# Optimization experiments

Measured on AMD Instinct MI355X. Metric: run time of the kernel, lower is better.

Reference implementation:

```python
import jax, jax.numpy as jnp
import numpy as np

B, N, K = 4, 512, 10
PI_SCALE = 0.05  # keeps sum_k pi in (0, 0.5) so the [1e-8, 1] clamp does not saturate at 1
MCMC_KEY = jax.random.key(42)


def setup_inputs() -> dict:
    key = jax.random.key(0)
    k1, k2, k3, k4 = jax.random.split(key, 4)
    mu = jax.random.normal(k1, (B, N, K), dtype=jnp.float32)
    sig = jax.random.uniform(k2, (B, N, K), dtype=jnp.float32)
    pi = jax.random.uniform(k3, (B, N, K), dtype=jnp.float32) * PI_SCALE
    A_0 = jax.random.uniform(k4, (N, N), dtype=jnp.float32)
    return {"mu": mu, "sig": sig, "pi": pi, "A_0": A_0, "num_samples": 100}


def reference(mu, sig, pi, A_0, num_samples):
    b, n, k = mu.shape

    # Mixture-weighted proposal mean/std:  sum_k softmax(pi)_k * {mu,sig}_k
    component_probs = jax.nn.softmax(pi, axis=-1)          # [B,N,K]
    selected_mu = jnp.sum(component_probs * mu, axis=-1)    # [B,N]
    selected_sig = jnp.sum(component_probs * sig, axis=-1)  # [B,N]

    # edge_probs[b,i,j] = clamp(sum_k pi[b,i,k]) -- constant in j; hoisted out of the loop
    # since it depends only on pi (the torch code recomputes it every step).
    edge_probs = jnp.clip(jnp.sum(pi, axis=2), 1e-8, 1.0)[:, :, None]  # [B,N,1]
    log_ep = jnp.log(edge_probs)                                        # [B,N,1]
    log_1mep = jnp.log(1.0 - edge_probs)                                # [B,N,1]

    def log_likelihood(A):  # A: [B,N,N] -> [N]  (sum over dims 0,1 as in torch)
        return jnp.sum(A * log_ep + (1.0 - A) * log_1mep, axis=(0, 1))

    def step(carry, t):
        current_A, acc = carry
        kk = jax.random.fold_in(MCMC_KEY, t)
        k_noise, k_unif = jax.random.split(kk)
        noise = jax.random.normal(k_noise, (b, n), dtype=selected_mu.dtype)
        proposed_mu = selected_mu + noise * selected_sig              # [B,N]
        # sigmoid of rank-1 outer product: einsum('bnc,bmc->bnm') with c==1
        proposed_A = jax.nn.sigmoid(proposed_mu[:, :, None] * proposed_mu[:, None, :])
        ratio = jnp.mean(jnp.clip(jnp.exp(log_likelihood(proposed_A) - log_likelihood(current_A)), 0.0, 1.0))
        accept = jax.random.uniform(k_unif, (b,)) < ratio             # [B] bool
        current_A = jnp.where(accept[:, None, None], proposed_A, current_A)
        return (current_A, acc + current_A), None

    cur0 = jnp.broadcast_to(A_0, (b, n, n)).astype(mu.dtype)
    acc0 = jnp.zeros((b, n, n), dtype=mu.dtype)
    (_, acc), _ = jax.lax.scan(step, (cur0, acc0), jnp.arange(num_samples))
    return acc / num_samples
```

## Files before the change

### kernel.cpp

```cpp
#include <hip/hip_runtime.h>
#include <stdint.h>

#define T_STEPS 100
#define BB 4
#define NN 512
#define KK 10
#define TBTOT (T_STEPS * BB)
#define LLT_ELT ((size_t)TBTOT * NN)

__device__ __forceinline__ uint32_t rotl32(uint32_t v, int d) {
  return (v << d) | (v >> (32 - d));
}

__device__ __forceinline__ void tf2x32(uint32_t k0, uint32_t k1,
                                       uint32_t& x0, uint32_t& x1) {
  uint32_t k2 = k0 ^ k1 ^ 0x1BD11BDAu;
  x0 += k0; x1 += k1;
#define TFR(r) { x0 += x1; x1 = rotl32(x1, r); x1 ^= x0; }
  TFR(13) TFR(15) TFR(26) TFR(6)   x0 += k1; x1 += k2 + 1u;
  TFR(17) TFR(29) TFR(16) TFR(24)  x0 += k2; x1 += k0 + 2u;
  TFR(13) TFR(15) TFR(26) TFR(6)   x0 += k0; x1 += k1 + 3u;
  TFR(17) TFR(29) TFR(16) TFR(24)  x0 += k1; x1 += k2 + 4u;
  TFR(13) TFR(15) TFR(26) TFR(6)   x0 += k2; x1 += k0 + 5u;
#undef TFR
}

__device__ __forceinline__ float bits_to_u01(uint32_t bits) {
  return __fsub_rn(__uint_as_float((bits >> 9) | 0x3f800000u), 1.0f);
}

__device__ __forceinline__ float erfinv_f32(float x) {
  float w = -logf(__fmul_rn(__fsub_rn(1.0f, x), __fadd_rn(1.0f, x)));
  float p;
  if (w < 5.0f) {
    w = __fsub_rn(w, 2.5f);
    p = 2.81022636e-08f;
    p = __fadd_rn(__fmul_rn(p, w), 3.43273939e-07f);
    p = __fadd_rn(__fmul_rn(p, w), -3.5233877e-06f);
    p = __fadd_rn(__fmul_rn(p, w), -4.39150654e-06f);
    p = __fadd_rn(__fmul_rn(p, w), 0.00021858087f);
    p = __fadd_rn(__fmul_rn(p, w), -0.00125372503f);
    p = __fadd_rn(__fmul_rn(p, w), -0.00417768164f);
    p = __fadd_rn(__fmul_rn(p, w), 0.246640727f);
    p = __fadd_rn(__fmul_rn(p, w), 1.50140941f);
  } else {
    w = __fsub_rn(sqrtf(w), 3.0f);
    p = -0.000200214257f;
    p = __fadd_rn(__fmul_rn(p, w), 0.000100950558f);
    p = __fadd_rn(__fmul_rn(p, w), 0.00134934322f);
    p = __fadd_rn(__fmul_rn(p, w), -0.00367342844f);
    p = __fadd_rn(__fmul_rn(p, w), 0.00573950773f);
    p = __fadd_rn(__fmul_rn(p, w), -0.0076224613f);
    p = __fadd_rn(__fmul_rn(p, w), 0.00943887047f);
    p = __fadd_rn(__fmul_rn(p, w), 1.00167406f);
    p = __fadd_rn(__fmul_rn(p, w), 2.83297682f);
  }
  return __fmul_rn(p, x);
}

__device__ __forceinline__ float fast_sigmoid(float x) {
  float e = __expf(-x);
  return __builtin_amdgcn_rcpf(__fadd_rn(1.0f, e));
}

template <int CTRL>
__device__ __forceinline__ float dpp_add(float x) {
  int v = __builtin_amdgcn_update_dpp(0, __float_as_int(x), CTRL, 0xF, 0xF, true);
  return __fadd_rn(x, __int_as_float(v));
}
__device__ __forceinline__ float readlane_f(float x, int lane) {
  return __int_as_float(__builtin_amdgcn_readlane(__float_as_int(x), lane));
}

__global__ void prep_kernel(const float* __restrict__ mu,
                            const float* __restrict__ sig,
                            const float* __restrict__ pi,
                            float* __restrict__ sm, float* __restrict__ ss,
                            float* __restrict__ Lf) {
  int m = blockIdx.x * blockDim.x + threadIdx.x;
  if (m >= BB * NN) return;
  const float* pp = pi + m * KK;
  float mx = pp[0];
  for (int k = 1; k < KK; k++) mx = fmaxf(mx, pp[k]);
  float e[KK]; float s = 0.0f;
  for (int k = 0; k < KK; k++) { e[k] = expf(__fsub_rn(pp[k], mx)); s = __fadd_rn(s, e[k]); }
  float smv = 0.0f, ssv = 0.0f, eps = 0.0f;
  for (int k = 0; k < KK; k++) {
    float p = e[k] / s;
    smv = __fadd_rn(smv, __fmul_rn(p, mu[m * KK + k]));
    ssv = __fadd_rn(ssv, __fmul_rn(p, sig[m * KK + k]));
    eps = __fadd_rn(eps, pp[k]);
  }
  sm[m] = smv; ss[m] = ssv;
  float ep = fminf(fmaxf(eps, 1e-8f), 1.0f);
  float lep = logf(ep);
  float l1 = logf(__fsub_rn(1.0f, ep));
  Lf[m] = (float)((double)lep - (double)l1);
}

__global__ void rng_kernel(const float* __restrict__ sm,
                           const float* __restrict__ ss,
                           float* __restrict__ pm, float* __restrict__ uacc) {
  int id = blockIdx.x * blockDim.x + threadIdx.x;
  if (id >= T_STEPS * BB * NN) return;
  int t = id >> 11;
  int m = id & 2047;

  uint32_t kk0 = 0u, kk1 = (uint32_t)t;
  tf2x32(0u, 42u, kk0, kk1);
  uint32_t n0 = 0u, n1 = 0u; tf2x32(kk0, kk1, n0, n1);
  uint32_t y0 = 0u, y1 = (uint32_t)m;
  tf2x32(n0, n1, y0, y1);
  uint32_t bits = y0 ^ y1;

  float u01 = bits_to_u01(bits);
  const float lo = -0.99999994f;
  float u = fmaxf(lo, __fadd_rn(__fmul_rn(u01, 2.0f), lo));
  float z = __fmul_rn(1.41421356237309515f, erfinv_f32(u));
  pm[id] = __fadd_rn(sm[m], __fmul_rn(z, ss[m]));

  if (m < 4) {
    uint32_t u0 = 0u, u1 = 1u; tf2x32(kk0, kk1, u0, u1);
    uint32_t c0 = 0u, c1 = (uint32_t)m;
    tf2x32(u0, u1, c0, c1);
    uacc[t * 4 + m] = bits_to_u01(c0 ^ c1);
  }
}

template <int SPLIT>
__global__ __launch_bounds__(512) void ll_kernel(const float* __restrict__ pm,
                                                 const float* __restrict__ Lf,
                                                 const float* __restrict__ A0,
                                                 double* __restrict__ llt_p,
                                                 double* __restrict__ ll0_p) {
  constexpr int CH = NN / SPLIT;
  __shared__ float spm[CH];
  __shared__ float sLc[CH];
  int j = threadIdx.x;
  int bi = blockIdx.x;
  if (bi < TBTOT * SPLIT) {
    int tb = bi / SPLIT;
    int s = bi - tb * SPLIT;
    int b = tb & 3;
    int i0 = s * CH;
    if (j < CH) {
      spm[j] = pm[tb * NN + i0 + j];
      sLc[j] = Lf[b * NN + i0 + j];
    }
    float pmj = pm[tb * NN + j];
    __syncthreads();
    double acc = 0.0;
    #pragma unroll 8
    for (int i = 0; i < CH; i += 2) {
      float x0 = __fmul_rn(spm[i], pmj);
      float x1 = __fmul_rn(spm[i + 1], pmj);
      float t0 = __fmul_rn(fast_sigmoid(x0), sLc[i]);
      float t1 = __fmul_rn(fast_sigmoid(x1), sLc[i + 1]);
      acc += (double)__fadd_rn(t0, t1);
    }
    llt_p[(size_t)s * LLT_ELT + (size_t)tb * NN + j] = acc;
  } else {
    int bi2 = bi - TBTOT * SPLIT;
    int b = bi2 / SPLIT;
    int s = bi2 - b * SPLIT;
    int i0 = s * CH;
    if (j < CH) sLc[j] = Lf[b * NN + i0 + j];
    __syncthreads();
    double acc = 0.0;
    #pragma unroll 4
    for (int i = 0; i < CH; i++) {
      acc += (double)A0[(size_t)(i0 + i) * NN + j] * (double)sLc[i];
    }
    ll0_p[s * (BB * NN) + b * NN + j] = acc;
  }
}

template <int SPLIT>
__global__ __launch_bounds__(512) void combine_kernel(const double* __restrict__ llt_p,
                                                      const double* __restrict__ ll0_p,
                                                      double* __restrict__ llt,
                                                      double* __restrict__ ll0,
                                                      double* __restrict__ tsum) {
  int bi = blockIdx.x;
  int j = threadIdx.x;
  if (bi < T_STEPS) {
    double tj = 0.0;
    #pragma unroll
    for (int b = 0; b < BB; b++) {
      size_t idx = ((size_t)bi * BB + b) * NN + j;
      double a = llt_p[idx];
      #pragma unroll
      for (int s = 1; s < SPLIT; s++) a += llt_p[(size_t)s * LLT_ELT + idx];
      llt[idx] = a;
      tj += a;
    }
    tsum[(size_t)bi * NN + j] = tj;
  } else {
    #pragma unroll
    for (int b = 0; b < BB; b++) {
      int idx = b * NN + j;
      double a = ll0_p[idx];
      #pragma unroll
      for (int s = 1; s < SPLIT; s++) a += ll0_p[s * (BB * NN) + idx];
      ll0[idx] = a;
    }
  }
}

struct ChainBuf {
  double2 ll[4][4];
  double2 ts[4];
};

#define CH_LOAD(BUF, T)                                                      \
  {                                                                          \
    _Pragma("unroll")                                                        \
    for (int b = 0; b < 4; b++) {                                            \
      _Pragma("unroll")                                                      \
      for (int k = 0; k < 4; k++)                                            \
        BUF.ll[b][k] = llt2[((size_t)(T) * 4 + b) * 256 + k * 64 + g];       \
    }                                                                        \
    _Pragma("unroll")                                                        \
    for (int k = 0; k < 4; k++)                                              \
      BUF.ts[k] = tsum2[(size_t)(T) * 256 + k * 64 + g];                     \
  }

#define CH_ACC(BUF, B)                                                       \
  {                                                                          \
    _Pragma("unroll")                                                        \
    for (int k = 0; k < 4; k++) {                                            \
      C[k].x += BUF.ll[B][k].x - cur[B][k].x;                                \
      C[k].y += BUF.ll[B][k].y - cur[B][k].y;                                \
      cur[B][k] = BUF.ll[B][k];                                              \
    }                                                                        \
  }

#define CH_STEP(BUF, T)                                                      \
  {                                                                          \
    float4 ua = sua[T];                                                      \
    float e0x = fminf(__expf((float)(BUF.ts[0].x - C[0].x)), 1.0f);          \
    float e0y = fminf(__expf((float)(BUF.ts[0].y - C[0].y)), 1.0f);          \
    float e1x = fminf(__expf((float)(BUF.ts[1].x - C[1].x)), 1.0f);          \
    float e1y = fminf(__expf((float)(BUF.ts[1].y - C[1].y)), 1.0f);          \
    float e2x = fminf(__expf((float)(BUF.ts[2].x - C[2].x)), 1.0f);          \
    float e2y = fminf(__expf((float)(BUF.ts[2].y - C[2].y)), 1.0f);          \
    float e3x = fminf(__expf((float)(BUF.ts[3].x - C[3].x)), 1.0f);          \
    float e3y = fminf(__expf((float)(BUF.ts[3].y - C[3].y)), 1.0f);          \
    float ps = __fadd_rn(__fadd_rn(__fadd_rn(e0x, e0y), __fadd_rn(e1x, e1y)),\
                         __fadd_rn(__fadd_rn(e2x, e2y), __fadd_rn(e3x, e3y)));\
    ps = dpp_add<0xB1>(ps);                 \
    ps = dpp_add<0x4E>(ps);                 \
    ps = dpp_add<0x141>(ps);     \
    ps = dpp_add<0x140>(ps);     \
    float s0 = readlane_f(ps, 0), s1 = readlane_f(ps, 16);                   \
    float s2 = readlane_f(ps, 32), s3 = readlane_f(ps, 48);                  \
    float tot = __fadd_rn(__fadd_rn(s0, s1), __fadd_rn(s2, s3));             \
    float ratio = __fmul_rn(tot, 1.0f / 512.0f);                             \
    if (ua.x < ratio) { st.x = (T); CH_ACC(BUF, 0) }                         \
    if (ua.y < ratio) { st.y = (T); CH_ACC(BUF, 1) }                         \
    if (ua.z < ratio) { st.z = (T); CH_ACC(BUF, 2) }                         \
    if (ua.w < ratio) { st.w = (T); CH_ACC(BUF, 3) }                         \
    if (g == 0) sst[T] = st;                                                 \
  }

__global__ __launch_bounds__(64) void chain_kernel(const double* __restrict__ llt,
                                                   const double* __restrict__ tsum,
                                                   const double* __restrict__ ll0,
                                                   const float* __restrict__ uacc,
                                                   int* __restrict__ counts) {
  __shared__ float4 sua[T_STEPS];
  __shared__ int4 sst[T_STEPS];
  __shared__ int scnt[BB * (T_STEPS + 1)];
  int g = threadIdx.x;

  const float4* uacc4 = (const float4*)uacc;
  for (int t = g; t < T_STEPS; t += 64) sua[t] = uacc4[t];

  const double2* llt2  = (const double2*)llt;
  const double2* tsum2 = (const double2*)tsum;
  const double2* ll02  = (const double2*)ll0;

  double2 cur[4][4];
  #pragma unroll
  for (int b = 0; b < 4; b++)
    #pragma unroll
    for (int k = 0; k < 4; k++) cur[b][k] = ll02[b * 256 + k * 64 + g];
  double2 C[4];
  #pragma unroll
  for (int k = 0; k < 4; k++) {
    C[k].x = (cur[0][k].x + cur[1][k].x) + (cur[2][k].x + cur[3][k].x);
    C[k].y = (cur[0][k].y + cur[1][k].y) + (cur[2][k].y + cur[3][k].y);
  }
  int4 st = make_int4(-1, -1, -1, -1);

  ChainBuf R0, R1, R2;
  CH_LOAD(R0, 0)
  CH_LOAD(R1, 1)
  CH_LOAD(R2, 2)
  __syncthreads();

  for (int t = 0; t < 99; t += 3) {
    CH_STEP(R0, t)
    CH_LOAD(R0, t + 3)
    CH_STEP(R1, t + 1)
    if (t + 4 < T_STEPS) CH_LOAD(R1, t + 4)
    CH_STEP(R2, t + 2)
    if (t + 5 < T_STEPS) CH_LOAD(R2, t + 5)
  }
  CH_STEP(R0, 99)

  __syncthreads();
  for (int s = g; s < BB * (T_STEPS + 1); s += 64) scnt[s] = 0;
  __syncthreads();
  for (int t = g; t < T_STEPS; t += 64) {
    int4 s4 = sst[t];
    atomicAdd(&scnt[0 * (T_STEPS + 1) + s4.x + 1], 1);
    atomicAdd(&scnt[1 * (T_STEPS + 1) + s4.y + 1], 1);
    atomicAdd(&scnt[2 * (T_STEPS + 1) + s4.z + 1], 1);
    atomicAdd(&scnt[3 * (T_STEPS + 1) + s4.w + 1], 1);
  }
  __syncthreads();
  for (int s = g; s < BB * (T_STEPS + 1); s += 64) counts[s] = scnt[s];
}

__global__ __launch_bounds__(512) void out_kernel(const float* __restrict__ pm,
                                                  const float* __restrict__ A0,
                                                  const int* __restrict__ counts,
                                                  float* __restrict__ out) {
  __shared__ int scnt[T_STEPS + 1];
  int b = blockIdx.x >> 9;
  int i = blockIdx.x & 511;
  int j = threadIdx.x;
  if (j < T_STEPS + 1) scnt[j] = counts[b * (T_STEPS + 1) + j];
  __syncthreads();
  float r = (float)scnt[0] * A0[(size_t)i * NN + j];
  #pragma unroll 4
  for (int t = 0; t < T_STEPS; t++) {
    int c = scnt[t + 1];
    if (c) {
      float x = __fmul_rn(pm[(size_t)(t * BB + b) * NN + i],
                          pm[(size_t)(t * BB + b) * NN + j]);
      r += (float)c * fast_sigmoid(x);
    }
  }
  out[((size_t)b * NN + i) * NN + j] = r * 0.01f;
}

extern "C" void kernel_launch(void* const* d_in, const int* in_sizes, int n_in,
                              void* d_out, int out_size, void* d_ws, size_t ws_size,
                              hipStream_t stream) {
  const float* mu  = (const float*)d_in[0];
  const float* sig = (const float*)d_in[1];
  const float* pi  = (const float*)d_in[2];
  const float* A0  = (const float*)d_in[3];

  char* ws = (char*)d_ws;
  size_t off = 0;
  auto alloc = [&](size_t bytes) -> char* {
    char* p = ws + off;
    off += (bytes + 255) & ~(size_t)255;
    return p;
  };
  double* llt  = (double*)alloc(LLT_ELT * 8);
  double* ll0  = (double*)alloc(BB * NN * 8);
  double* tsum = (double*)alloc((size_t)T_STEPS * NN * 8);
  float*  pm   = (float*)alloc(LLT_ELT * 4);
  float*  Lf   = (float*)alloc(BB * NN * 4);
  float*  sm   = (float*)alloc(BB * NN * 4);
  float*  ssv  = (float*)alloc(BB * NN * 4);
  float*  uacc = (float*)alloc(T_STEPS * 4 * 4);
  int*    cnts = (int*)alloc(BB * (T_STEPS + 1) * 4);
  size_t fixed_end = off;
  float*  outp = (float*)d_out;

  size_t part4 = 4 * LLT_ELT * 8 + 4 * BB * NN * 8 + 1024;
  size_t part2 = 2 * LLT_ELT * 8 + 2 * BB * NN * 8 + 1024;
  int split = (ws_size >= fixed_end + part4) ? 4
            : (ws_size >= fixed_end + part2) ? 2 : 1;

  double* llt_p;
  double* ll0_p;
  if (split > 1) {
    llt_p = (double*)alloc((size_t)split * LLT_ELT * 8);
    ll0_p = (double*)alloc((size_t)split * BB * NN * 8);
  } else {
    llt_p = llt;
    ll0_p = ll0;
  }

  prep_kernel<<<8, 256, 0, stream>>>(mu, sig, pi, sm, ssv, Lf);
  rng_kernel<<<(T_STEPS * BB * NN + 255) / 256, 256, 0, stream>>>(sm, ssv, pm, uacc);
  if (split == 4) {
    ll_kernel<4><<<(TBTOT + BB) * 4, 512, 0, stream>>>(pm, Lf, A0, llt_p, ll0_p);
    combine_kernel<4><<<T_STEPS + 1, 512, 0, stream>>>(llt_p, ll0_p, llt, ll0, tsum);
  } else if (split == 2) {
    ll_kernel<2><<<(TBTOT + BB) * 2, 512, 0, stream>>>(pm, Lf, A0, llt_p, ll0_p);
    combine_kernel<2><<<T_STEPS + 1, 512, 0, stream>>>(llt_p, ll0_p, llt, ll0, tsum);
  } else {
    ll_kernel<1><<<TBTOT + BB, 512, 0, stream>>>(pm, Lf, A0, llt_p, ll0_p);
    combine_kernel<1><<<T_STEPS + 1, 512, 0, stream>>>(llt_p, ll0_p, llt, ll0, tsum);
  }
  chain_kernel<<<1, 64, 0, stream>>>(llt, tsum, ll0, uacc, cnts);
  out_kernel<<<BB * NN, 512, 0, stream>>>(pm, A0, cnts, outp);
}
```

Baseline: 154.1 us.

## Store per-step log-likelihoods as float and derive totals inside chain kernel

Log-likelihood partials and combined values are now stored as float instead of double. The separate tsum array is removed; the chain kernel instead computes per-column totals on the fly from the four batch values. The split==1 path also skips the combine kernel, since ll_kernel already writes straight into llt/ll0. This halves the memory traffic of the serial single-wavefront chain kernel and of combine, at the cost of float rounding in the stored likelihoods, which could flip accept decisions near the threshold.

```diff
diff --git a/kernel.cpp b/kernel.cpp
--- a/kernel.cpp
+++ b/kernel.cpp
@@ -7,6 +7,8 @@
 #define KK 10
 #define TBTOT (T_STEPS * BB)
 #define LLT_ELT ((size_t)TBTOT * NN)
+
+typedef float f4 __attribute__((ext_vector_type(4)));
 
 __device__ __forceinline__ uint32_t rotl32(uint32_t v, int d) {
   return (v << d) | (v >> (32 - d));
@@ -131,8 +133,8 @@
 __global__ __launch_bounds__(512) void ll_kernel(const float* __restrict__ pm,
                                                  const float* __restrict__ Lf,
                                                  const float* __restrict__ A0,
-                                                 double* __restrict__ llt_p,
-                                                 double* __restrict__ ll0_p) {
+                                                 float* __restrict__ llt_p,
+                                                 float* __restrict__ ll0_p) {
   constexpr int CH = NN / SPLIT;
   __shared__ float spm[CH];
   __shared__ float sLc[CH];
@@ -158,7 +160,7 @@
       float t1 = __fmul_rn(fast_sigmoid(x1), sLc[i + 1]);
       acc += (double)__fadd_rn(t0, t1);
     }
-    llt_p[(size_t)s * LLT_ELT + (size_t)tb * NN + j] = acc;
+    llt_p[(size_t)s * LLT_ELT + (size_t)tb * NN + j] = (float)acc;
   } else {
     int bi2 = bi - TBTOT * SPLIT;
     int b = bi2 / SPLIT;
@@ -171,101 +173,90 @@
     for (int i = 0; i < CH; i++) {
       acc += (double)A0[(size_t)(i0 + i) * NN + j] * (double)sLc[i];
     }
-    ll0_p[s * (BB * NN) + b * NN + j] = acc;
+    ll0_p[s * (BB * NN) + b * NN + j] = (float)acc;
   }
 }
 
 template <int SPLIT>
-__global__ __launch_bounds__(512) void combine_kernel(const double* __restrict__ llt_p,
-                                                      const double* __restrict__ ll0_p,
-                                                      double* __restrict__ llt,
-                                                      double* __restrict__ ll0,
-                                                      double* __restrict__ tsum) {
+__global__ __launch_bounds__(512) void combine_kernel(const float* __restrict__ llt_p,
+                                                      const float* __restrict__ ll0_p,
+                                                      float* __restrict__ llt,
+                                                      float* __restrict__ ll0) {
   int bi = blockIdx.x;
   int j = threadIdx.x;
   if (bi < T_STEPS) {
-    double tj = 0.0;
     #pragma unroll
     for (int b = 0; b < BB; b++) {
       size_t idx = ((size_t)bi * BB + b) * NN + j;
-      double a = llt_p[idx];
+      double a = (double)llt_p[idx];
       #pragma unroll
-      for (int s = 1; s < SPLIT; s++) a += llt_p[(size_t)s * LLT_ELT + idx];
-      llt[idx] = a;
-      tj += a;
-    }
-    tsum[(size_t)bi * NN + j] = tj;
+      for (int s = 1; s < SPLIT; s++) a += (double)llt_p[(size_t)s * LLT_ELT + idx];
+      llt[idx] = (float)a;
+    }
   } else {
     #pragma unroll
     for (int b = 0; b < BB; b++) {
       int idx = b * NN + j;
-      double a = ll0_p[idx];
+      double a = (double)ll0_p[idx];
       #pragma unroll
-      for (int s = 1; s < SPLIT; s++) a += ll0_p[s * (BB * NN) + idx];
-      ll0[idx] = a;
-    }
-  }
-}
-
-struct ChainBuf {
-  double2 ll[4][4];
-  double2 ts[4];
-};
-
-#define CH_LOAD(BUF, T)                                                      \
+      for (int s = 1; s < SPLIT; s++) a += (double)ll0_p[s * (BB * NN) + idx];
+      ll0[idx] = (float)a;
+    }
+  }
+}
+
+#define CH_LOADF(BUF, T)                                                     \
   {                                                                          \
     _Pragma("unroll")                                                        \
     for (int b = 0; b < 4; b++) {                                            \
       _Pragma("unroll")                                                      \
-      for (int k = 0; k < 4; k++)                                            \
-        BUF.ll[b][k] = llt2[((size_t)(T) * 4 + b) * 256 + k * 64 + g];       \
+      for (int k = 0; k < 2; k++)                                            \
+        BUF[b][k] = llt4[(((size_t)(T) * 4 + b) * 2 + k) * 64 + g];          \
     }                                                                        \
-    _Pragma("unroll")                                                        \
-    for (int k = 0; k < 4; k++)                                              \
-      BUF.ts[k] = tsum2[(size_t)(T) * 256 + k * 64 + g];                     \
-  }
-
-#define CH_ACC(BUF, B)                                                       \
+  }
+
+#define CH_ACCF(BUF, B)                                                      \
   {                                                                          \
     _Pragma("unroll")                                                        \
-    for (int k = 0; k < 4; k++) {                                            \
-      C[k].x += BUF.ll[B][k].x - cur[B][k].x;                                \
-      C[k].y += BUF.ll[B][k].y - cur[B][k].y;                                \
-      cur[B][k] = BUF.ll[B][k];                                              \
+    for (int k = 0; k < 2; k++) {                                            \
+      _Pragma("unroll")                                                      \
+      for (int c = 0; c < 4; c++)                                            \
+        C[k][c] += (double)BUF[B][k][c] - (double)cur[B][k][c];              \
+      cur[B][k] = BUF[B][k];                                                 \
     }                                                                        \
   }
 
-#define CH_STEP(BUF, T)                                                      \
+#define CH_STEPF(BUF, T)                                                     \
   {                                                                          \
     float4 ua = sua[T];                                                      \
-    float e0x = fminf(__expf((float)(BUF.ts[0].x - C[0].x)), 1.0f);          \
-    float e0y = fminf(__expf((float)(BUF.ts[0].y - C[0].y)), 1.0f);          \
-    float e1x = fminf(__expf((float)(BUF.ts[1].x - C[1].x)), 1.0f);          \
-    float e1y = fminf(__expf((float)(BUF.ts[1].y - C[1].y)), 1.0f);          \
-    float e2x = fminf(__expf((float)(BUF.ts[2].x - C[2].x)), 1.0f);          \
-    float e2y = fminf(__expf((float)(BUF.ts[2].y - C[2].y)), 1.0f);          \
-    float e3x = fminf(__expf((float)(BUF.ts[3].x - C[3].x)), 1.0f);          \
-    float e3y = fminf(__expf((float)(BUF.ts[3].y - C[3].y)), 1.0f);          \
-    float ps = __fadd_rn(__fadd_rn(__fadd_rn(e0x, e0y), __fadd_rn(e1x, e1y)),\
-                         __fadd_rn(__fadd_rn(e2x, e2y), __fadd_rn(e3x, e3y)));\
+    float ps = 0.0f;                                                         \
+    _Pragma("unroll")                                                        \
+    for (int k = 0; k < 2; k++) {                                            \
+      _Pragma("unroll")                                                      \
+      for (int c = 0; c < 4; c++) {                                          \
+        double ts = ((double)BUF[0][k][c] + (double)BUF[1][k][c]) +          \
+                    ((double)BUF[2][k][c] + (double)BUF[3][k][c]);           \
+        float e = fminf(__expf((float)(ts - C[k][c])), 1.0f);                \
+        ps = __fadd_rn(ps, e);                                               \
+      }                                                                      \
+    }                                                                        \
     ps = dpp_add<0xB1>(ps);                 \
     ps = dpp_add<0x4E>(ps);                 \
-    ps = dpp_add<0x141>(ps);     \
-    ps = dpp_add<0x140>(ps);     \
+    ps = dpp_add<0x141>(ps);        \
+    ps = dpp_add<0x140>(ps);        \
     float s0 = readlane_f(ps, 0), s1 = readlane_f(ps, 16);                   \
     float s2 = readlane_f(ps, 32), s3 = readlane_f(ps, 48);                  \
     float tot = __fadd_rn(__fadd_rn(s0, s1), __fadd_rn(s2, s3));             \
     float ratio = __fmul_rn(tot, 1.0f / 512.0f);                             \
-    if (ua.x < ratio) { st.x = (T); CH_ACC(BUF, 0) }                         \
-    if (ua.y < ratio) { st.y = (T); CH_ACC(BUF, 1) }                         \
-    if (ua.z < ratio) { st.z = (T); CH_ACC(BUF, 2) }                         \
-    if (ua.w < ratio) { st.w = (T); CH_ACC(BUF, 3) }                         \
+    if (ua.x < ratio) { st.x = (T); CH_ACCF(BUF, 0) }                        \
+    if (ua.y < ratio) { st.y = (T); CH_ACCF(BUF, 1) }                        \
+    if (ua.z < ratio) { st.z = (T); CH_ACCF(BUF, 2) }                        \
+    if (ua.w < ratio) { st.w = (T); CH_ACCF(BUF, 3) }                        \
     if (g == 0) sst[T] = st;                                                 \
   }
 
-__global__ __launch_bounds__(64) void chain_kernel(const double* __restrict__ llt,
-                                                   const double* __restrict__ tsum,
-                                                   const double* __restrict__ ll0,
+__global__ __launch_bounds__(64) void chain_kernel(const float* __restrict__ llt,
+                                                   const float* __restrict__ ll0,
                                                    const float* __restrict__ uacc,
                                                    int* __restrict__ counts) {
   __shared__ float4 sua[T_STEPS];
@@ -276,38 +267,38 @@
   const float4* uacc4 = (const float4*)uacc;
   for (int t = g; t < T_STEPS; t += 64) sua[t] = uacc4[t];
 
-  const double2* llt2  = (const double2*)llt;
-  const double2* tsum2 = (const double2*)tsum;
-  const double2* ll02  = (const double2*)ll0;
-
-  double2 cur[4][4];
+  const f4* llt4 = (const f4*)llt;
+  const f4* ll04 = (const f4*)ll0;
+
+  f4 cur[4][2];
   #pragma unroll
   for (int b = 0; b < 4; b++)
     #pragma unroll
-    for (int k = 0; k < 4; k++) cur[b][k] = ll02[b * 256 + k * 64 + g];
-  double2 C[4];
+    for (int k = 0; k < 2; k++) cur[b][k] = ll04[(b * 2 + k) * 64 + g];
+  double C[2][4];
   #pragma unroll
-  for (int k = 0; k < 4; k++) {
-    C[k].x = (cur[0][k].x + cur[1][k].x) + (cur[2][k].x + cur[3][k].x);
-    C[k].y = (cur[0][k].y + cur[1][k].y) + (cur[2][k].y + cur[3][k].y);
-  }
+  for (int k = 0; k < 2; k++)
+    #pragma unroll
+    for (int c = 0; c < 4; c++)
+      C[k][c] = ((double)cur[0][k][c] + (double)cur[1][k][c]) +
+                ((double)cur[2][k][c] + (double)cur[3][k][c]);
   int4 st = make_int4(-1, -1, -1, -1);
 
-  ChainBuf R0, R1, R2;
-  CH_LOAD(R0, 0)
-  CH_LOAD(R1, 1)
-  CH_LOAD(R2, 2)
+  f4 R0[4][2], R1[4][2], R2[4][2];
+  CH_LOADF(R0, 0)
+  CH_LOADF(R1, 1)
+  CH_LOADF(R2, 2)
   __syncthreads();
 
   for (int t = 0; t < 99; t += 3) {
-    CH_STEP(R0, t)
-    CH_LOAD(R0, t + 3)
-    CH_STEP(R1, t + 1)
-    if (t + 4 < T_STEPS) CH_LOAD(R1, t + 4)
-    CH_STEP(R2, t + 2)
-    if (t + 5 < T_STEPS) CH_LOAD(R2, t + 5)
-  }
-  CH_STEP(R0, 99)
+    CH_STEPF(R0, t)
+    CH_LOADF(R0, t + 3)
+    CH_STEPF(R1, t + 1)
+    if (t + 4 < T_STEPS) CH_LOADF(R1, t + 4)
+    CH_STEPF(R2, t + 2)
+    if (t + 5 < T_STEPS) CH_LOADF(R2, t + 5)
+  }
+  CH_STEPF(R0, 99)
 
   __syncthreads();
   for (int s = g; s < BB * (T_STEPS + 1); s += 64) scnt[s] = 0;
@@ -361,28 +352,27 @@
     off += (bytes + 255) & ~(size_t)255;
     return p;
   };
-  double* llt  = (double*)alloc(LLT_ELT * 8);
-  double* ll0  = (double*)alloc(BB * NN * 8);
-  double* tsum = (double*)alloc((size_t)T_STEPS * NN * 8);
-  float*  pm   = (float*)alloc(LLT_ELT * 4);
-  float*  Lf   = (float*)alloc(BB * NN * 4);
-  float*  sm   = (float*)alloc(BB * NN * 4);
-  float*  ssv  = (float*)alloc(BB * NN * 4);
-  float*  uacc = (float*)alloc(T_STEPS * 4 * 4);
-  int*    cnts = (int*)alloc(BB * (T_STEPS + 1) * 4);
+  float* llt  = (float*)alloc(LLT_ELT * 4);
+  float* ll0  = (float*)alloc(BB * NN * 4);
+  float* pm   = (float*)alloc(LLT_ELT * 4);
+  float* Lf   = (float*)alloc(BB * NN * 4);
+  float* sm   = (float*)alloc(BB * NN * 4);
+  float* ssv  = (float*)alloc(BB * NN * 4);
+  float* uacc = (float*)alloc(T_STEPS * 4 * 4);
+  int*   cnts = (int*)alloc(BB * (T_STEPS + 1) * 4);
   size_t fixed_end = off;
-  float*  outp = (float*)d_out;
-
-  size_t part4 = 4 * LLT_ELT * 8 + 4 * BB * NN * 8 + 1024;
-  size_t part2 = 2 * LLT_ELT * 8 + 2 * BB * NN * 8 + 1024;
+  float* outp = (float*)d_out;
+
+  size_t part4 = 4 * LLT_ELT * 4 + 4 * BB * NN * 4 + 1024;
+  size_t part2 = 2 * LLT_ELT * 4 + 2 * BB * NN * 4 + 1024;
   int split = (ws_size >= fixed_end + part4) ? 4
             : (ws_size >= fixed_end + part2) ? 2 : 1;
 
-  double* llt_p;
-  double* ll0_p;
+  float* llt_p;
+  float* ll0_p;
   if (split > 1) {
-    llt_p = (double*)alloc((size_t)split * LLT_ELT * 8);
-    ll0_p = (double*)alloc((size_t)split * BB * NN * 8);
+    llt_p = (float*)alloc((size_t)split * LLT_ELT * 4);
+    ll0_p = (float*)alloc((size_t)split * BB * NN * 4);
   } else {
     llt_p = llt;
     ll0_p = ll0;
@@ -392,14 +382,13 @@
   rng_kernel<<<(T_STEPS * BB * NN + 255) / 256, 256, 0, stream>>>(sm, ssv, pm, uacc);
   if (split == 4) {
     ll_kernel<4><<<(TBTOT + BB) * 4, 512, 0, stream>>>(pm, Lf, A0, llt_p, ll0_p);
-    combine_kernel<4><<<T_STEPS + 1, 512, 0, stream>>>(llt_p, ll0_p, llt, ll0, tsum);
+    combine_kernel<4><<<T_STEPS + 1, 512, 0, stream>>>(llt_p, ll0_p, llt, ll0);
   } else if (split == 2) {
     ll_kernel<2><<<(TBTOT + BB) * 2, 512, 0, stream>>>(pm, Lf, A0, llt_p, ll0_p);
-    combine_kernel<2><<<T_STEPS + 1, 512, 0, stream>>>(llt_p, ll0_p, llt, ll0, tsum);
+    combine_kernel<2><<<T_STEPS + 1, 512, 0, stream>>>(llt_p, ll0_p, llt, ll0);
   } else {
     ll_kernel<1><<<TBTOT + BB, 512, 0, stream>>>(pm, Lf, A0, llt_p, ll0_p);
-    combine_kernel<1><<<T_STEPS + 1, 512, 0, stream>>>(llt_p, ll0_p, llt, ll0, tsum);
-  }
-  chain_kernel<<<1, 64, 0, stream>>>(llt, tsum, ll0, uacc, cnts);
+  }
+  chain_kernel<<<1, 64, 0, stream>>>(llt, ll0, uacc, cnts);
   out_kernel<<<BB * NN, 512, 0, stream>>>(pm, A0, cnts, outp);
 }
```

Measured after the change: 147.8 us. 4.1% less time.
